# Performance work log

Measured on AMD Instinct MI355X. Metric: run time of the kernel, lower is better.

The kernel has to match this reference:

```python
import jax, jax.numpy as jnp
import numpy as np

D_MODEL = 1024
NUM_HEADS = 16
HEAD_DIM = D_MODEL // NUM_HEADS
SCALE = HEAD_DIM ** -0.5


def setup_inputs() -> dict:
    key = jax.random.key(0)
    k1, k2, k3 = jax.random.split(key, 3)
    B, N = 2, 2048
    x = jax.random.normal(k1, (B, N, D_MODEL), dtype=jnp.float32)
    w_qkv = jax.random.normal(k2, (D_MODEL, 3 * D_MODEL), dtype=jnp.float32) * (D_MODEL ** -0.5)
    b_qkv = jnp.zeros((3 * D_MODEL,), dtype=jnp.float32)
    w_proj = jax.random.normal(k3, (D_MODEL, D_MODEL), dtype=jnp.float32) * (D_MODEL ** -0.5)
    b_proj = jnp.zeros((D_MODEL,), dtype=jnp.float32)
    return {"x": x, "w_qkv": w_qkv, "b_qkv": b_qkv, "w_proj": w_proj, "b_proj": b_proj}


def reference(x, w_qkv, b_qkv, w_proj, b_proj):
    B, N, C = x.shape
    H, Hd = NUM_HEADS, HEAD_DIM
    # fused QKV projection: [B,N,3C] -> [3,B,H,N,Hd]
    qkv = (x @ w_qkv + b_qkv).reshape(B, N, 3, H, Hd).transpose(2, 0, 3, 1, 4)
    q, k, v = qkv[0], qkv[1], qkv[2]
    # manual scaled dot-product attention (full NxN scores, as in source)
    attn = jnp.einsum('bhqd,bhkd->bhqk', q, k) * SCALE
    attn = jax.nn.softmax(attn, axis=-1)
    out = jnp.einsum('bhqk,bhkd->bhqd', attn, v)  # [B,H,N,Hd]
    out = out.transpose(0, 2, 1, 3).reshape(B, N, C)
    return out @ w_proj + b_proj
```

## Files before the change

### kernel.cpp

```cpp
#include <hip/hip_runtime.h>
#include <hip/hip_bf16.h>
#include <stdint.h>

typedef __attribute__((ext_vector_type(8))) __bf16 bf16x8;
typedef __attribute__((ext_vector_type(4))) __bf16 bf16x4;
typedef __attribute__((ext_vector_type(4))) float f32x4;

#define AS1 __attribute__((address_space(1)))
#define AS3 __attribute__((address_space(3)))

__device__ __forceinline__ void load_lds16(const void* g, void* l) {
    __builtin_amdgcn_global_load_lds((const AS1 void*)g, (AS3 void*)l, 16, 0, 0);
}

__device__ __forceinline__ float m3(float a, float b, float c) {
    return fmaxf(fmaxf(a, b), c);
}

constexpr float QSCALE = 0.18033688011112042f;

__device__ __forceinline__ int sigma32(int kv) {
    return (kv < 16) ? ((kv >> 2) * 8 + (kv & 3))
                     : (((kv - 16) >> 2) * 8 + 4 + ((kv - 16) & 3));
}

__global__ void cvt_x(const float4* __restrict__ x, bf16x4* __restrict__ o, int n4) {
    int i = blockIdx.x * blockDim.x + threadIdx.x;
    if (i >= n4) return;
    float4 v = x[i];
    bf16x4 r;
    r[0] = (__bf16)v.x; r[1] = (__bf16)v.y; r[2] = (__bf16)v.z; r[3] = (__bf16)v.w;
    o[i] = r;
}

__global__ void tconv(const float* __restrict__ src, __bf16* __restrict__ dst,
                      int R, int C) {
    __shared__ float tile[32][33];
    int c0 = blockIdx.x * 32, r0 = blockIdx.y * 32;
    int tx = threadIdx.x, ty = threadIdx.y;
    #pragma unroll
    for (int i = 0; i < 32; i += 8)
        tile[ty + i][tx] = src[(size_t)(r0 + ty + i) * C + c0 + tx];
    __syncthreads();
    #pragma unroll
    for (int i = 0; i < 32; i += 8)
        dst[(size_t)(c0 + ty + i) * R + r0 + tx] = (__bf16)tile[tx][ty + i];
}

template <int MODE>
__global__ __launch_bounds__(256)
void gemm128(const __bf16* __restrict__ A, const __bf16* __restrict__ Bt,
             const float* __restrict__ bias, void* __restrict__ outp,
             int M, int Nn, int K) {
    __shared__ __bf16 As[3][128][32];
    __shared__ __bf16 Bs[3][128][32];
    const int t = threadIdx.x;
    const int w = t >> 6, l = t & 63;
    const int lrow = l & 15, lhi = l >> 4;
    const int wr = (w >> 1) * 64, wc = (w & 1) * 64;

    int nwg = gridDim.x * gridDim.y;
    int flat = blockIdx.x + blockIdx.y * gridDim.x;
    if ((nwg & 7) == 0) flat = (flat & 7) * (nwg >> 3) + (flat >> 3);
    const int m0 = (flat / gridDim.x) * 128;
    const int n0 = (flat % gridDim.x) * 128;

    f32x4 acc[4][4] = {};

    const int sr = t >> 2;
    const int dc = (t & 3) * 8;
    const int scsw = ((t & 3) ^ ((sr >> 1) & 3)) * 8;
    const __bf16* agb = A + (size_t)(m0 + sr) * K + scsw;
    const __bf16* bgb = Bt + (size_t)(n0 + sr) * K + scsw;

#define STAGE_G(BUF, KT)                                                   \
    { load_lds16(agb + (KT), &As[BUF][sr][dc]);                            \
      load_lds16(agb + (size_t)64 * K + (KT), &As[BUF][64 + sr][dc]);      \
      load_lds16(bgb + (KT), &Bs[BUF][sr][dc]);                            \
      load_lds16(bgb + (size_t)64 * K + (KT), &Bs[BUF][64 + sr][dc]); }

    STAGE_G(0, 0)
    STAGE_G(1, 32)

    const int rofs = (lhi ^ ((lrow >> 1) & 3)) << 4;
    const int nt = K >> 5;
    int cur = 0, pre = 2;
    for (int tt = 0; tt < nt; ++tt) {
        if (tt + 2 < nt) {
            STAGE_G(pre, (tt + 2) * 32)
            asm volatile("s_waitcnt vmcnt(8)" ::: "memory");
        } else if (tt + 1 < nt) {
            asm volatile("s_waitcnt vmcnt(4)" ::: "memory");
        } else {
            asm volatile("s_waitcnt vmcnt(0)" ::: "memory");
        }
        __builtin_amdgcn_sched_barrier(0);
        __builtin_amdgcn_s_barrier();
        __builtin_amdgcn_sched_barrier(0);

        bf16x8 af[4], bfv[4];
        #pragma unroll
        for (int i = 0; i < 4; ++i)
            af[i] = *(const bf16x8*)((const char*)&As[cur][wr + i * 16 + lrow][0] + rofs);
        #pragma unroll
        for (int j = 0; j < 4; ++j)
            bfv[j] = *(const bf16x8*)((const char*)&Bs[cur][wc + j * 16 + lrow][0] + rofs);
        __builtin_amdgcn_s_setprio(1);
        #pragma unroll
        for (int i = 0; i < 4; ++i)
            #pragma unroll
            for (int j = 0; j < 4; ++j)
                acc[i][j] = __builtin_amdgcn_mfma_f32_16x16x32_bf16(
                    af[i], bfv[j], acc[i][j], 0, 0, 0);
        __builtin_amdgcn_s_setprio(0);

        __builtin_amdgcn_sched_barrier(0);
        asm volatile("s_waitcnt lgkmcnt(0)" ::: "memory");
        __builtin_amdgcn_s_barrier();
        __builtin_amdgcn_sched_barrier(0);

        cur = (cur == 2) ? 0 : cur + 1;
        pre = (pre == 2) ? 0 : pre + 1;
    }
#undef STAGE_G

    #pragma unroll
    for (int i = 0; i < 4; ++i)
        #pragma unroll
        for (int j = 0; j < 4; ++j)
            #pragma unroll
            for (int r = 0; r < 4; ++r) {
                int row = m0 + wr + i * 16 + lhi * 4 + r;
                int col = n0 + wc + j * 16 + lrow;
                float val = acc[i][j][r] + bias[col];
                if (MODE == 0) {
                    int which = col >> 10;
                    int h = (col >> 6) & 15;
                    int d = col & 63;
                    int b = row >> 11;
                    int n = row & 2047;
                    int bh = (b << 4) + h;
                    if (which == 2) {
                        ((__bf16*)outp)[(size_t)2 * (32 * 2048 * 64) +
                                        ((size_t)bh * 64 + d) * 2048 +
                                        (n & ~31) + sigma32(n & 31)] = (__bf16)val;
                    } else {
                        if (which == 0) val *= QSCALE;
                        ((__bf16*)outp)[(size_t)which * (32 * 2048 * 64) +
                                        ((size_t)bh * 2048 + n) * 64 + d] = (__bf16)val;
                    }
                } else {
                    ((float*)outp)[(size_t)row * Nn + col] = val;
                }
            }
}

__global__ __launch_bounds__(256)
void attn_fwd(const __bf16* __restrict__ q, const __bf16* __restrict__ k,
              const __bf16* __restrict__ vt, __bf16* __restrict__ out) {
    __shared__ __bf16 KsV[2][64][64];
    __shared__ __bf16 VsV[2][64][64];
    char* ksB = (char*)KsV;
    char* vsB = (char*)VsV;

    const int t = threadIdx.x;
    const int w = t >> 6, l = t & 63;
    const int lrow = l & 15, lhi = l >> 4;
    const int bh = blockIdx.y;
    const int q0 = blockIdx.x * 128 + w * 32;

    const __bf16* qp = q + ((size_t)bh * 2048 + q0) * 64;
    bf16x8 qfA0 = *(const bf16x8*)(qp + lrow * 64 + lhi * 8);
    bf16x8 qfA1 = *(const bf16x8*)(qp + lrow * 64 + 32 + lhi * 8);
    bf16x8 qfB0 = *(const bf16x8*)(qp + (16 + lrow) * 64 + lhi * 8);
    bf16x8 qfB1 = *(const bf16x8*)(qp + (16 + lrow) * 64 + 32 + lhi * 8);

    f32x4 oA[4] = {}, oB[4] = {};
    float mA = -1e30f, mB = -1e30f;
    float lA = 0.f, lB = 0.f;

    const __bf16* kg = k + (size_t)bh * 2048 * 64;
    const __bf16* vg = vt + (size_t)bh * 64 * 2048;

    const int sr = t >> 3;
    const int sw8 = ((t & 7) ^ (sr & 7)) * 8;
    const int rsw = (lrow & 7) << 4;

    {
        char* kd = ksB + t * 16;
        char* vd = vsB + t * 16;
        load_lds16(kg + (size_t)sr * 64 + sw8, kd);
        load_lds16(kg + (size_t)(32 + sr) * 64 + sw8, kd + 4096);
        load_lds16(vg + (size_t)sr * 2048 + sw8, vd);
        load_lds16(vg + (size_t)(32 + sr) * 2048 + sw8, vd + 4096);
    }

    const __bf16* kst  = kg + (size_t)(64 + sr) * 64 + sw8;
    const __bf16* kst2 = kst + 32 * 64;
    const __bf16* vst  = vg + (size_t)sr * 2048 + 64 + sw8;
    const __bf16* vst2 = vst + 32 * 2048;

    int cur = 0;
    for (int kv0 = 0; kv0 < 2048; kv0 += 64) {
        __syncthreads();
        if (kv0 + 64 < 2048) {
            char* kd = ksB + (cur ^ 1) * 8192 + t * 16;
            char* vd = vsB + (cur ^ 1) * 8192 + t * 16;
            load_lds16(kst, kd);
            load_lds16(kst2, kd + 4096);
            load_lds16(vst, vd);
            load_lds16(vst2, vd + 4096);
            kst += 4096; kst2 += 4096; vst += 64; vst2 += 64;
        }
        const char* kb = ksB + cur * 8192 + lrow * 128;
        const char* vb = vsB + cur * 8192 + lrow * 128;
        const int o0 = (lhi << 4) ^ rsw;
        const int o4 = ((4 + lhi) << 4) ^ rsw;

        f32x4 sA0 = {}, sA1 = {}, sA2 = {}, sA3 = {};
        f32x4 sB0 = {}, sB1 = {}, sB2 = {}, sB3 = {};
        __builtin_amdgcn_s_setprio(1);
        {
            bf16x8 kf0, kf1;
#define QK_GROUP(SA, SB, BASE)                                                 \
            kf0 = *(const bf16x8*)(kb + (BASE) + o0);                          \
            kf1 = *(const bf16x8*)(kb + (BASE) + o4);                          \
            SA = __builtin_amdgcn_mfma_f32_16x16x32_bf16(kf0, qfA0, SA, 0, 0, 0); \
            SA = __builtin_amdgcn_mfma_f32_16x16x32_bf16(kf1, qfA1, SA, 0, 0, 0); \
            SB = __builtin_amdgcn_mfma_f32_16x16x32_bf16(kf0, qfB0, SB, 0, 0, 0); \
            SB = __builtin_amdgcn_mfma_f32_16x16x32_bf16(kf1, qfB1, SB, 0, 0, 0);
            QK_GROUP(sA0, sB0, 0)
            QK_GROUP(sA1, sB1, 2048)
            QK_GROUP(sA2, sB2, 4096)
            QK_GROUP(sA3, sB3, 6144)
#undef QK_GROUP
        }
        __builtin_amdgcn_s_setprio(0);

        float u0 = m3(sA0[0], sA0[1], sA0[2]);
        float u1 = m3(sA0[3], sA1[0], sA1[1]);
        float u2 = m3(sA1[2], sA1[3], sA2[0]);
        float u3 = m3(sA2[1], sA2[2], sA2[3]);
        float u4 = m3(sA3[0], sA3[1], sA3[2]);
        float tmA = fmaxf(m3(u0, u1, u2), m3(u3, u4, sA3[3]));
        float v0 = m3(sB0[0], sB0[1], sB0[2]);
        float v1 = m3(sB0[3], sB1[0], sB1[1]);
        float v2 = m3(sB1[2], sB1[3], sB2[0]);
        float v3 = m3(sB2[1], sB2[2], sB2[3]);
        float v4 = m3(sB3[0], sB3[1], sB3[2]);
        float tmB = fmaxf(m3(v0, v1, v2), m3(v3, v4, sB3[3]));
        tmA = fmaxf(tmA, __shfl_xor(tmA, 16, 64));
        tmA = fmaxf(tmA, __shfl_xor(tmA, 32, 64));
        tmB = fmaxf(tmB, __shfl_xor(tmB, 16, 64));
        tmB = fmaxf(tmB, __shfl_xor(tmB, 32, 64));
        if (!__all(tmA <= mA + 8.0f && tmB <= mB + 8.0f)) {
            float mnA = fmaxf(mA, tmA), mnB = fmaxf(mB, tmB);
            float cA = __builtin_amdgcn_exp2f(mA - mnA);
            float cB = __builtin_amdgcn_exp2f(mB - mnB);
            lA *= cA; lB *= cB;
            #pragma unroll
            for (int dt = 0; dt < 4; ++dt)
                #pragma unroll
                for (int r = 0; r < 4; ++r) { oA[dt][r] *= cA; oB[dt][r] *= cB; }
            mA = mnA; mB = mnB;
        }
        float pA[16], pB[16];
        #pragma unroll
        for (int r = 0; r < 4; ++r) {
            pA[r]      = __builtin_amdgcn_exp2f(sA0[r] - mA);
            pA[4 + r]  = __builtin_amdgcn_exp2f(sA1[r] - mA);
            pA[8 + r]  = __builtin_amdgcn_exp2f(sA2[r] - mA);
            pA[12 + r] = __builtin_amdgcn_exp2f(sA3[r] - mA);
            pB[r]      = __builtin_amdgcn_exp2f(sB0[r] - mB);
            pB[4 + r]  = __builtin_amdgcn_exp2f(sB1[r] - mB);
            pB[8 + r]  = __builtin_amdgcn_exp2f(sB2[r] - mB);
            pB[12 + r] = __builtin_amdgcn_exp2f(sB3[r] - mB);
        }
        float rsA = 0.f, rsB = 0.f;
        #pragma unroll
        for (int j = 0; j < 16; ++j) { rsA += pA[j]; rsB += pB[j]; }
        lA += rsA; lB += rsB;

        bf16x8 pfA0, pfA1, pfB0, pfB1;
        #pragma unroll
        for (int j = 0; j < 8; ++j) {
            pfA0[j] = (__bf16)pA[j]; pfA1[j] = (__bf16)pA[8 + j];
            pfB0[j] = (__bf16)pB[j]; pfB1[j] = (__bf16)pB[8 + j];
        }

        __builtin_amdgcn_s_setprio(1);
        #pragma unroll
        for (int dt = 0; dt < 4; ++dt) {
            bf16x8 vf0 = *(const bf16x8*)(vb + dt * 2048 + o0);
            bf16x8 vf1 = *(const bf16x8*)(vb + dt * 2048 + o4);
            oA[dt] = __builtin_amdgcn_mfma_f32_16x16x32_bf16(vf0, pfA0, oA[dt], 0, 0, 0);
            oA[dt] = __builtin_amdgcn_mfma_f32_16x16x32_bf16(vf1, pfA1, oA[dt], 0, 0, 0);
            oB[dt] = __builtin_amdgcn_mfma_f32_16x16x32_bf16(vf0, pfB0, oB[dt], 0, 0, 0);
            oB[dt] = __builtin_amdgcn_mfma_f32_16x16x32_bf16(vf1, pfB1, oB[dt], 0, 0, 0);
        }
        __builtin_amdgcn_s_setprio(0);
        cur ^= 1;
    }

    lA += __shfl_xor(lA, 16, 64); lA += __shfl_xor(lA, 32, 64);
    lB += __shfl_xor(lB, 16, 64); lB += __shfl_xor(lB, 32, 64);
    float invA = __builtin_amdgcn_rcpf(lA);
    float invB = __builtin_amdgcn_rcpf(lB);

    const int b = bh >> 4, h = bh & 15;
    __bf16* orowA = out + ((size_t)(b * 2048 + q0 + lrow)) * 1024 + h * 64;
    __bf16* orowB = out + ((size_t)(b * 2048 + q0 + 16 + lrow)) * 1024 + h * 64;
    #pragma unroll
    for (int dt = 0; dt < 4; ++dt) {
        bf16x4 ovA, ovB;
        #pragma unroll
        for (int r = 0; r < 4; ++r) {
            ovA[r] = (__bf16)(oA[dt][r] * invA);
            ovB[r] = (__bf16)(oB[dt][r] * invB);
        }
        *(bf16x4*)(orowA + dt * 16 + lhi * 4) = ovA;
        *(bf16x4*)(orowB + dt * 16 + lhi * 4) = ovB;
    }
}

extern "C" void kernel_launch(void* const* d_in, const int* in_sizes, int n_in,
                              void* d_out, int out_size, void* d_ws, size_t ws_size,
                              hipStream_t stream) {
    const float* x      = (const float*)d_in[0];
    const float* w_qkv  = (const float*)d_in[1];
    const float* b_qkv  = (const float*)d_in[2];
    const float* w_proj = (const float*)d_in[3];
    const float* b_proj = (const float*)d_in[4];
    float* out = (float*)d_out;

    __bf16* ws     = (__bf16*)d_ws;
    __bf16* x_bf   = ws;
    __bf16* wqkvT  = x_bf + 4096 * 1024;
    __bf16* wprojT = wqkvT + 3072 * 1024;
    __bf16* qb     = wprojT + 1024 * 1024;
    __bf16* kb     = qb + 32 * 2048 * 64;
    __bf16* vtb    = kb + 32 * 2048 * 64;
    __bf16* attn   = vtb + 32 * 2048 * 64;

    cvt_x<<<4096, 256, 0, stream>>>((const float4*)x, (bf16x4*)x_bf, 4096 * 1024 / 4);
    tconv<<<dim3(96, 32), dim3(32, 8), 0, stream>>>(w_qkv, wqkvT, 1024, 3072);
    tconv<<<dim3(32, 32), dim3(32, 8), 0, stream>>>(w_proj, wprojT, 1024, 1024);
    gemm128<0><<<dim3(24, 32), 256, 0, stream>>>(x_bf, wqkvT, b_qkv, qb, 4096, 3072, 1024);
    attn_fwd<<<dim3(16, 32), 256, 0, stream>>>(qb, kb, vtb, attn);
    gemm128<1><<<dim3(8, 32), 256, 0, stream>>>(attn, wprojT, b_proj, out, 4096, 1024, 1024);
}
```

Before: 208.5 us.

## Fuse prep kernels, remap GEMM tile order, double attention KV stage size

Merges the x conversion and both weight transpose kernels into one launch, which removes two kernel launch gaps. Replaces the GEMM workgroup remap with a chunked mapping meant to give better L2 locality across XCDs. Doubles the attention K/V stage to 128 keys per barrier, which halves the number of syncs and issues larger prefetches, at the cost of twice the LDS per block (64KB), which may lower occupancy.

```diff
diff --git a/kernel.cpp b/kernel.cpp
--- a/kernel.cpp
+++ b/kernel.cpp
@@ -24,20 +24,11 @@
                      : (((kv - 16) >> 2) * 8 + 4 + ((kv - 16) & 3));
 }
 
-__global__ void cvt_x(const float4* __restrict__ x, bf16x4* __restrict__ o, int n4) {
-    int i = blockIdx.x * blockDim.x + threadIdx.x;
-    if (i >= n4) return;
-    float4 v = x[i];
-    bf16x4 r;
-    r[0] = (__bf16)v.x; r[1] = (__bf16)v.y; r[2] = (__bf16)v.z; r[3] = (__bf16)v.w;
-    o[i] = r;
-}
-
-__global__ void tconv(const float* __restrict__ src, __bf16* __restrict__ dst,
-                      int R, int C) {
+__device__ __forceinline__ void tconv_body(const float* __restrict__ src,
+                                           __bf16* __restrict__ dst,
+                                           int R, int C, int c0, int r0, int t) {
     __shared__ float tile[32][33];
-    int c0 = blockIdx.x * 32, r0 = blockIdx.y * 32;
-    int tx = threadIdx.x, ty = threadIdx.y;
+    const int tx = t & 31, ty = t >> 5;
     #pragma unroll
     for (int i = 0; i < 32; i += 8)
         tile[ty + i][tx] = src[(size_t)(r0 + ty + i) * C + c0 + tx];
@@ -45,6 +36,33 @@
     #pragma unroll
     for (int i = 0; i < 32; i += 8)
         dst[(size_t)(c0 + ty + i) * R + r0 + tx] = (__bf16)tile[tx][ty + i];
+}
+
+__global__ __launch_bounds__(256)
+void prep(const float* __restrict__ x, const float* __restrict__ w_qkv,
+          const float* __restrict__ w_proj, __bf16* __restrict__ x_bf,
+          __bf16* __restrict__ wqkvT, __bf16* __restrict__ wprojT) {
+    const int bid = blockIdx.x;
+    const int t = threadIdx.x;
+    if (bid < 1024) {
+        const float4* xv = (const float4*)x;
+        bf16x4* ov = (bf16x4*)x_bf;
+        int i = bid * 256 + t;
+        #pragma unroll
+        for (int it = 0; it < 4; ++it, i += 262144) {
+            float4 v = xv[i];
+            bf16x4 r;
+            r[0] = (__bf16)v.x; r[1] = (__bf16)v.y;
+            r[2] = (__bf16)v.z; r[3] = (__bf16)v.w;
+            ov[i] = r;
+        }
+    } else if (bid < 1024 + 3072) {
+        const int b = bid - 1024;
+        tconv_body(w_qkv, wqkvT, 1024, 3072, (b % 96) * 32, (b / 96) * 32, t);
+    } else {
+        const int b = bid - 4096;
+        tconv_body(w_proj, wprojT, 1024, 1024, (b & 31) * 32, (b >> 5) * 32, t);
+    }
 }
 
 template <int MODE>
@@ -59,11 +77,19 @@
     const int lrow = l & 15, lhi = l >> 4;
     const int wr = (w >> 1) * 64, wc = (w & 1) * 64;
 
-    int nwg = gridDim.x * gridDim.y;
-    int flat = blockIdx.x + blockIdx.y * gridDim.x;
-    if ((nwg & 7) == 0) flat = (flat & 7) * (nwg >> 3) + (flat >> 3);
-    const int m0 = (flat / gridDim.x) * 128;
-    const int n0 = (flat % gridDim.x) * 128;
+    int m0, n0;
+    {
+        const int f = blockIdx.x + blockIdx.y * gridDim.x;
+        if ((gridDim.y & 3) == 0 && (gridDim.x & 1) == 0) {
+            const int c = f & 7, i = f >> 3;
+            const int nch = gridDim.x >> 1;
+            const int mrow = i / nch, ncol = i % nch;
+            m0 = ((c & 3) * (gridDim.y >> 2) + mrow) * 128;
+            n0 = ((c >> 2) * nch + ncol) * 128;
+        } else {
+            m0 = blockIdx.y * 128; n0 = blockIdx.x * 128;
+        }
+    }
 
     f32x4 acc[4][4] = {};
 
@@ -158,8 +184,8 @@
 __global__ __launch_bounds__(256)
 void attn_fwd(const __bf16* __restrict__ q, const __bf16* __restrict__ k,
               const __bf16* __restrict__ vt, __bf16* __restrict__ out) {
-    __shared__ __bf16 KsV[2][64][64];
-    __shared__ __bf16 VsV[2][64][64];
+    __shared__ __bf16 KsV[2][2][64][64];
+    __shared__ __bf16 VsV[2][2][64][64];
     char* ksB = (char*)KsV;
     char* vsB = (char*)VsV;
 
@@ -191,114 +217,123 @@
         char* vd = vsB + t * 16;
         load_lds16(kg + (size_t)sr * 64 + sw8, kd);
         load_lds16(kg + (size_t)(32 + sr) * 64 + sw8, kd + 4096);
+        load_lds16(kg + (size_t)(64 + sr) * 64 + sw8, kd + 8192);
+        load_lds16(kg + (size_t)(96 + sr) * 64 + sw8, kd + 12288);
         load_lds16(vg + (size_t)sr * 2048 + sw8, vd);
         load_lds16(vg + (size_t)(32 + sr) * 2048 + sw8, vd + 4096);
-    }
-
-    const __bf16* kst  = kg + (size_t)(64 + sr) * 64 + sw8;
-    const __bf16* kst2 = kst + 32 * 64;
-    const __bf16* vst  = vg + (size_t)sr * 2048 + 64 + sw8;
-    const __bf16* vst2 = vst + 32 * 2048;
+        load_lds16(vg + (size_t)sr * 2048 + 64 + sw8, vd + 8192);
+        load_lds16(vg + (size_t)(32 + sr) * 2048 + 64 + sw8, vd + 12288);
+    }
+
+    const __bf16* kst = kg + (size_t)(128 + sr) * 64 + sw8;
+    const __bf16* vst = vg + (size_t)sr * 2048 + 128 + sw8;
 
     int cur = 0;
-    for (int kv0 = 0; kv0 < 2048; kv0 += 64) {
+    for (int kv0 = 0; kv0 < 2048; kv0 += 128) {
         __syncthreads();
-        if (kv0 + 64 < 2048) {
-            char* kd = ksB + (cur ^ 1) * 8192 + t * 16;
-            char* vd = vsB + (cur ^ 1) * 8192 + t * 16;
+        if (kv0 + 128 < 2048) {
+            char* kd = ksB + (cur ^ 1) * 16384 + t * 16;
+            char* vd = vsB + (cur ^ 1) * 16384 + t * 16;
             load_lds16(kst, kd);
-            load_lds16(kst2, kd + 4096);
+            load_lds16(kst + 32 * 64, kd + 4096);
+            load_lds16(kst + 64 * 64, kd + 8192);
+            load_lds16(kst + 96 * 64, kd + 12288);
             load_lds16(vst, vd);
-            load_lds16(vst2, vd + 4096);
-            kst += 4096; kst2 += 4096; vst += 64; vst2 += 64;
-        }
-        const char* kb = ksB + cur * 8192 + lrow * 128;
-        const char* vb = vsB + cur * 8192 + lrow * 128;
-        const int o0 = (lhi << 4) ^ rsw;
-        const int o4 = ((4 + lhi) << 4) ^ rsw;
-
-        f32x4 sA0 = {}, sA1 = {}, sA2 = {}, sA3 = {};
-        f32x4 sB0 = {}, sB1 = {}, sB2 = {}, sB3 = {};
-        __builtin_amdgcn_s_setprio(1);
-        {
-            bf16x8 kf0, kf1;
+            load_lds16(vst + 32 * 2048, vd + 4096);
+            load_lds16(vst + 64, vd + 8192);
+            load_lds16(vst + 32 * 2048 + 64, vd + 12288);
+            kst += 8192; vst += 128;
+        }
+        #pragma unroll
+        for (int h = 0; h < 2; ++h) {
+            const char* kb = ksB + cur * 16384 + h * 8192 + lrow * 128;
+            const char* vb = vsB + cur * 16384 + h * 8192 + lrow * 128;
+            const int o0 = (lhi << 4) ^ rsw;
+            const int o4 = ((4 + lhi) << 4) ^ rsw;
+
+            f32x4 sA0 = {}, sA1 = {}, sA2 = {}, sA3 = {};
+            f32x4 sB0 = {}, sB1 = {}, sB2 = {}, sB3 = {};
+            __builtin_amdgcn_s_setprio(1);
+            {
+                bf16x8 kf0, kf1;
 #define QK_GROUP(SA, SB, BASE)                                                 \
-            kf0 = *(const bf16x8*)(kb + (BASE) + o0);                          \
-            kf1 = *(const bf16x8*)(kb + (BASE) + o4);                          \
-            SA = __builtin_amdgcn_mfma_f32_16x16x32_bf16(kf0, qfA0, SA, 0, 0, 0); \
-            SA = __builtin_amdgcn_mfma_f32_16x16x32_bf16(kf1, qfA1, SA, 0, 0, 0); \
-            SB = __builtin_amdgcn_mfma_f32_16x16x32_bf16(kf0, qfB0, SB, 0, 0, 0); \
-            SB = __builtin_amdgcn_mfma_f32_16x16x32_bf16(kf1, qfB1, SB, 0, 0, 0);
-            QK_GROUP(sA0, sB0, 0)
-            QK_GROUP(sA1, sB1, 2048)
-            QK_GROUP(sA2, sB2, 4096)
-            QK_GROUP(sA3, sB3, 6144)
+                kf0 = *(const bf16x8*)(kb + (BASE) + o0);                      \
+                kf1 = *(const bf16x8*)(kb + (BASE) + o4);                      \
+                SA = __builtin_amdgcn_mfma_f32_16x16x32_bf16(kf0, qfA0, SA, 0, 0, 0); \
+                SA = __builtin_amdgcn_mfma_f32_16x16x32_bf16(kf1, qfA1, SA, 0, 0, 0); \
+                SB = __builtin_amdgcn_mfma_f32_16x16x32_bf16(kf0, qfB0, SB, 0, 0, 0); \
+                SB = __builtin_amdgcn_mfma_f32_16x16x32_bf16(kf1, qfB1, SB, 0, 0, 0);
+                QK_GROUP(sA0, sB0, 0)
+                QK_GROUP(sA1, sB1, 2048)
+                QK_GROUP(sA2, sB2, 4096)
+                QK_GROUP(sA3, sB3, 6144)
 #undef QK_GROUP
-        }
-        __builtin_amdgcn_s_setprio(0);
-
-        float u0 = m3(sA0[0], sA0[1], sA0[2]);
-        float u1 = m3(sA0[3], sA1[0], sA1[1]);
-        float u2 = m3(sA1[2], sA1[3], sA2[0]);
-        float u3 = m3(sA2[1], sA2[2], sA2[3]);
-        float u4 = m3(sA3[0], sA3[1], sA3[2]);
-        float tmA = fmaxf(m3(u0, u1, u2), m3(u3, u4, sA3[3]));
-        float v0 = m3(sB0[0], sB0[1], sB0[2]);
-        float v1 = m3(sB0[3], sB1[0], sB1[1]);
-        float v2 = m3(sB1[2], sB1[3], sB2[0]);
-        float v3 = m3(sB2[1], sB2[2], sB2[3]);
-        float v4 = m3(sB3[0], sB3[1], sB3[2]);
-        float tmB = fmaxf(m3(v0, v1, v2), m3(v3, v4, sB3[3]));
-        tmA = fmaxf(tmA, __shfl_xor(tmA, 16, 64));
-        tmA = fmaxf(tmA, __shfl_xor(tmA, 32, 64));
-        tmB = fmaxf(tmB, __shfl_xor(tmB, 16, 64));
-        tmB = fmaxf(tmB, __shfl_xor(tmB, 32, 64));
-        if (!__all(tmA <= mA + 8.0f && tmB <= mB + 8.0f)) {
-            float mnA = fmaxf(mA, tmA), mnB = fmaxf(mB, tmB);
-            float cA = __builtin_amdgcn_exp2f(mA - mnA);
-            float cB = __builtin_amdgcn_exp2f(mB - mnB);
-            lA *= cA; lB *= cB;
-            #pragma unroll
-            for (int dt = 0; dt < 4; ++dt)
+            }
+            __builtin_amdgcn_s_setprio(0);
+
+            float u0 = m3(sA0[0], sA0[1], sA0[2]);
+            float u1 = m3(sA0[3], sA1[0], sA1[1]);
+            float u2 = m3(sA1[2], sA1[3], sA2[0]);
+            float u3 = m3(sA2[1], sA2[2], sA2[3]);
+            float u4 = m3(sA3[0], sA3[1], sA3[2]);
+            float tmA = fmaxf(m3(u0, u1, u2), m3(u3, u4, sA3[3]));
+            float v0 = m3(sB0[0], sB0[1], sB0[2]);
+            float v1 = m3(sB0[3], sB1[0], sB1[1]);
+            float v2 = m3(sB1[2], sB1[3], sB2[0]);
+            float v3 = m3(sB2[1], sB2[2], sB2[3]);
+            float v4 = m3(sB3[0], sB3[1], sB3[2]);
+            float tmB = fmaxf(m3(v0, v1, v2), m3(v3, v4, sB3[3]));
+            tmA = fmaxf(tmA, __shfl_xor(tmA, 16, 64));
+            tmA = fmaxf(tmA, __shfl_xor(tmA, 32, 64));
+            tmB = fmaxf(tmB, __shfl_xor(tmB, 16, 64));
+            tmB = fmaxf(tmB, __shfl_xor(tmB, 32, 64));
+            if (!__all(tmA <= mA + 8.0f && tmB <= mB + 8.0f)) {
+                float mnA = fmaxf(mA, tmA), mnB = fmaxf(mB, tmB);
+                float cA = __builtin_amdgcn_exp2f(mA - mnA);
+                float cB = __builtin_amdgcn_exp2f(mB - mnB);
+                lA *= cA; lB *= cB;
                 #pragma unroll
-                for (int r = 0; r < 4; ++r) { oA[dt][r] *= cA; oB[dt][r] *= cB; }
-            mA = mnA; mB = mnB;
-        }
-        float pA[16], pB[16];
-        #pragma unroll
-        for (int r = 0; r < 4; ++r) {
-            pA[r]      = __builtin_amdgcn_exp2f(sA0[r] - mA);
-            pA[4 + r]  = __builtin_amdgcn_exp2f(sA1[r] - mA);
-            pA[8 + r]  = __builtin_amdgcn_exp2f(sA2[r] - mA);
-            pA[12 + r] = __builtin_amdgcn_exp2f(sA3[r] - mA);
-            pB[r]      = __builtin_amdgcn_exp2f(sB0[r] - mB);
-            pB[4 + r]  = __builtin_amdgcn_exp2f(sB1[r] - mB);
-            pB[8 + r]  = __builtin_amdgcn_exp2f(sB2[r] - mB);
-            pB[12 + r] = __builtin_amdgcn_exp2f(sB3[r] - mB);
-        }
-        float rsA = 0.f, rsB = 0.f;
-        #pragma unroll
-        for (int j = 0; j < 16; ++j) { rsA += pA[j]; rsB += pB[j]; }
-        lA += rsA; lB += rsB;
-
-        bf16x8 pfA0, pfA1, pfB0, pfB1;
-        #pragma unroll
-        for (int j = 0; j < 8; ++j) {
-            pfA0[j] = (__bf16)pA[j]; pfA1[j] = (__bf16)pA[8 + j];
-            pfB0[j] = (__bf16)pB[j]; pfB1[j] = (__bf16)pB[8 + j];
-        }
-
-        __builtin_amdgcn_s_setprio(1);
-        #pragma unroll
-        for (int dt = 0; dt < 4; ++dt) {
-            bf16x8 vf0 = *(const bf16x8*)(vb + dt * 2048 + o0);
-            bf16x8 vf1 = *(const bf16x8*)(vb + dt * 2048 + o4);
-            oA[dt] = __builtin_amdgcn_mfma_f32_16x16x32_bf16(vf0, pfA0, oA[dt], 0, 0, 0);
-            oA[dt] = __builtin_amdgcn_mfma_f32_16x16x32_bf16(vf1, pfA1, oA[dt], 0, 0, 0);
-            oB[dt] = __builtin_amdgcn_mfma_f32_16x16x32_bf16(vf0, pfB0, oB[dt], 0, 0, 0);
-            oB[dt] = __builtin_amdgcn_mfma_f32_16x16x32_bf16(vf1, pfB1, oB[dt], 0, 0, 0);
-        }
-        __builtin_amdgcn_s_setprio(0);
+                for (int dt = 0; dt < 4; ++dt)
+                    #pragma unroll
+                    for (int r = 0; r < 4; ++r) { oA[dt][r] *= cA; oB[dt][r] *= cB; }
+                mA = mnA; mB = mnB;
+            }
+            float pA[16], pB[16];
+            #pragma unroll
+            for (int r = 0; r < 4; ++r) {
+                pA[r]      = __builtin_amdgcn_exp2f(sA0[r] - mA);
+                pA[4 + r]  = __builtin_amdgcn_exp2f(sA1[r] - mA);
+                pA[8 + r]  = __builtin_amdgcn_exp2f(sA2[r] - mA);
+                pA[12 + r] = __builtin_amdgcn_exp2f(sA3[r] - mA);
+                pB[r]      = __builtin_amdgcn_exp2f(sB0[r] - mB);
+                pB[4 + r]  = __builtin_amdgcn_exp2f(sB1[r] - mB);
+                pB[8 + r]  = __builtin_amdgcn_exp2f(sB2[r] - mB);
+                pB[12 + r] = __builtin_amdgcn_exp2f(sB3[r] - mB);
+            }
+            float rsA = 0.f, rsB = 0.f;
+            #pragma unroll
+            for (int j = 0; j < 16; ++j) { rsA += pA[j]; rsB += pB[j]; }
+            lA += rsA; lB += rsB;
+
+            bf16x8 pfA0, pfA1, pfB0, pfB1;
+            #pragma unroll
+            for (int j = 0; j < 8; ++j) {
+                pfA0[j] = (__bf16)pA[j]; pfA1[j] = (__bf16)pA[8 + j];
+                pfB0[j] = (__bf16)pB[j]; pfB1[j] = (__bf16)pB[8 + j];
+            }
+
+            __builtin_amdgcn_s_setprio(1);
+            #pragma unroll
+            for (int dt = 0; dt < 4; ++dt) {
+                bf16x8 vf0 = *(const bf16x8*)(vb + dt * 2048 + o0);
+                bf16x8 vf1 = *(const bf16x8*)(vb + dt * 2048 + o4);
+                oA[dt] = __builtin_amdgcn_mfma_f32_16x16x32_bf16(vf0, pfA0, oA[dt], 0, 0, 0);
+                oA[dt] = __builtin_amdgcn_mfma_f32_16x16x32_bf16(vf1, pfA1, oA[dt], 0, 0, 0);
+                oB[dt] = __builtin_amdgcn_mfma_f32_16x16x32_bf16(vf0, pfB0, oB[dt], 0, 0, 0);
+                oB[dt] = __builtin_amdgcn_mfma_f32_16x16x32_bf16(vf1, pfB1, oB[dt], 0, 0, 0);
+            }
+            __builtin_amdgcn_s_setprio(0);
+        }
         cur ^= 1;
     }
 
@@ -342,9 +377,7 @@
     __bf16* vtb    = kb + 32 * 2048 * 64;
     __bf16* attn   = vtb + 32 * 2048 * 64;
 
-    cvt_x<<<4096, 256, 0, stream>>>((const float4*)x, (bf16x4*)x_bf, 4096 * 1024 / 4);
-    tconv<<<dim3(96, 32), dim3(32, 8), 0, stream>>>(w_qkv, wqkvT, 1024, 3072);
-    tconv<<<dim3(32, 32), dim3(32, 8), 0, stream>>>(w_proj, wprojT, 1024, 1024);
+    prep<<<5120, 256, 0, stream>>>(x, w_qkv, w_proj, x_bf, wqkvT, wprojT);
     gemm128<0><<<dim3(24, 32), 256, 0, stream>>>(x_bf, wqkvT, b_qkv, qb, 4096, 3072, 1024);
     attn_fwd<<<dim3(16, 32), 256, 0, stream>>>(qb, kb, vtb, attn);
     gemm128<1><<<dim3(8, 32), 256, 0, stream>>>(attn, wprojT, b_proj, out, 4096, 1024, 1024);
```

New measurement: 204.6 us. Within noise of the previous version (-1.9%).
